# Kernel tuning notes

Hardware: AMD Instinct MI355X
Metric: run time of the kernel (lower is better)

The kernel has to match this reference:

```python
import jax, jax.numpy as jnp
import numpy as np

HID, H, KV, D = 2048, 16, 4, 128
B, L = 8, 1024
T = B * L
EPS = 1e-6
NEG = -1e9


def _rms(x, w):
    # RMSNorm over head_dim in fp32
    var = jnp.mean(x.astype(jnp.float32) ** 2, axis=-1, keepdims=True)
    return (x.astype(jnp.float32) * jax.lax.rsqrt(var + EPS)).astype(x.dtype) * w


def _rot_half(x):
    x1, x2 = jnp.split(x, 2, axis=-1)
    return jnp.concatenate([-x2, x1], axis=-1)


def setup_inputs() -> dict:
    key = jax.random.key(0)
    ks = jax.random.split(key, 24)
    inp = {}
    inp['packed_sequence'] = jax.random.normal(ks[0], (T, HID), jnp.float32) * 0.02
    # RoPE tables: positions restart per sample
    pos = jnp.tile(jnp.arange(L, dtype=jnp.float32), B)  # [T]
    inv_freq = 1.0 / (10000.0 ** (jnp.arange(0, D, 2, dtype=jnp.float32) / D))
    ang = pos[:, None] * inv_freq[None, :]  # [T, D/2]
    inp['cos'] = jnp.concatenate([jnp.cos(ang), jnp.cos(ang)], axis=-1)
    inp['sin'] = jnp.concatenate([jnp.sin(ang), jnp.sin(ang)], axis=-1)
    # per-sample causal additive mask [B, L, L]
    causal = jnp.tril(jnp.ones((L, L), bool))
    inp['attn_bias'] = jnp.broadcast_to(jnp.where(causal, 0.0, NEG).astype(jnp.float32), (B, L, L))
    inp['gen_mask'] = jax.random.randint(ks[1], (T,), 0, 2, jnp.int32)
    s = 0.02
    inp['Wq'] = jax.random.normal(ks[2], (H * D, HID), jnp.float32) * s
    inp['bq'] = jnp.zeros((H * D,), jnp.float32)
    inp['Wqg'] = jax.random.normal(ks[3], (H * D, HID), jnp.float32) * s
    inp['bqg'] = jnp.zeros((H * D,), jnp.float32)
    inp['Wk'] = jax.random.normal(ks[4], (KV * D, HID), jnp.float32) * s
    inp['bk'] = jnp.zeros((KV * D,), jnp.float32)
    inp['Wkg'] = jax.random.normal(ks[5], (KV * D, HID), jnp.float32) * s
    inp['bkg'] = jnp.zeros((KV * D,), jnp.float32)
    inp['Wv'] = jax.random.normal(ks[6], (KV * D, HID), jnp.float32) * s
    inp['bv'] = jnp.zeros((KV * D,), jnp.float32)
    inp['Wvg'] = jax.random.normal(ks[7], (KV * D, HID), jnp.float32) * s
    inp['bvg'] = jnp.zeros((KV * D,), jnp.float32)
    inp['Wo'] = jax.random.normal(ks[8], (HID, H * D), jnp.float32) * s
    inp['Wog'] = jax.random.normal(ks[9], (HID, H * D), jnp.float32) * s
    inp['q_norm_w'] = jnp.ones((D,), jnp.float32)
    inp['q_norm_gen_w'] = jnp.ones((D,), jnp.float32)
    inp['k_norm_w'] = jnp.ones((D,), jnp.float32)
    inp['k_norm_gen_w'] = jnp.ones((D,), jnp.float32)
    return inp


def reference(packed_sequence, cos, sin, attn_bias, gen_mask,
              Wq, bq, Wqg, bqg, Wk, bk, Wkg, bkg, Wv, bv, Wvg, bvg,
              Wo, Wog, q_norm_w, q_norm_gen_w, k_norm_w, k_norm_gen_w):
    route = (gen_mask > 0)[:, None]  # [T,1]; und/gen indexes partition tokens -> select
    # dual-path QKV projections (scatter into zero buffers == per-token select)
    q = jnp.where(route, packed_sequence @ Wqg.T + bqg, packed_sequence @ Wq.T + bq)
    k = jnp.where(route, packed_sequence @ Wkg.T + bkg, packed_sequence @ Wk.T + bk)
    v = jnp.where(route, packed_sequence @ Wvg.T + bvg, packed_sequence @ Wv.T + bv)
    q = q.reshape(T, H, D)
    k = k.reshape(T, KV, D)
    v = v.reshape(T, KV, D)
    rh = route[:, :, None]  # [T,1,1]
    # dual-path per-head-dim RMSNorm
    q = jnp.where(rh, _rms(q, q_norm_gen_w), _rms(q, q_norm_w))
    k = jnp.where(rh, _rms(k, k_norm_gen_w), _rms(k, k_norm_w))
    # RoPE (broadcast over heads, unsqueeze_dim=1)
    c, s = cos[:, None, :], sin[:, None, :]
    q = q * c + _rot_half(q) * s
    k = k * c + _rot_half(k) * s
    # GQA: repeat kv heads to H
    k = jnp.repeat(k, H // KV, axis=1)
    v = jnp.repeat(v, H // KV, axis=1)
    # ragged attention, equal sample lens -> batched SDPA with per-sample masks
    qb = q.reshape(B, L, H, D)
    kb = k.reshape(B, L, H, D)
    vb = v.reshape(B, L, H, D)
    scores = jnp.einsum('blhd,bmhd->bhlm', qb, kb) / np.sqrt(D).astype(np.float32)
    scores = scores + attn_bias[:, None, :, :]
    p = jax.nn.softmax(scores, axis=-1)
    o = jnp.einsum('bhlm,bmhd->blhd', p, vb).reshape(T, H * D)
    # dual-path output projection (no bias)
    return jnp.where(route, o @ Wog.T, o @ Wo.T)
```

## Files before the change

### kernel.cpp

```cpp
#include <hip/hip_runtime.h>

#define T_TOK 8192
#define HID   2048
#define NH    16
#define NKV   4
#define HD    128

typedef __attribute__((ext_vector_type(8))) short short8;
typedef __attribute__((ext_vector_type(4))) float f32x4;
typedef __attribute__((ext_vector_type(4))) unsigned short us4;

__device__ __forceinline__ unsigned short f2b(float f) {
  union { float f; unsigned int u; } x; x.f = f;
  unsigned int u = x.u;
  return (unsigned short)((u + 0x7FFFu + ((u >> 16) & 1u)) >> 16);
}
__device__ __forceinline__ float b2f(unsigned short u) {
  union { float f; unsigned int u; } x; x.u = ((unsigned int)u) << 16; return x.f;
}

__device__ __forceinline__ void ld_lds16(const unsigned short* g, unsigned short* l) {
  __builtin_amdgcn_global_load_lds(
      (const __attribute__((address_space(1))) unsigned int*)g,
      (__attribute__((address_space(3))) unsigned int*)l, 16, 0, 0);
}

__global__ __launch_bounds__(1024) void scan_route(const int* __restrict__ gm,
                                                   int* __restrict__ perm,
                                                   int* __restrict__ n0p) {
  __shared__ int cnt[1024];
  int tid = threadIdx.x;
  int base = tid * 8;
  int r[8]; int c0 = 0;
#pragma unroll
  for (int i = 0; i < 8; i++) { r[i] = gm[base + i] > 0 ? 1 : 0; c0 += 1 - r[i]; }
  cnt[tid] = c0;
  __syncthreads();
  for (int off = 1; off < 1024; off <<= 1) {
    int add = (tid >= off) ? cnt[tid - off] : 0;
    __syncthreads();
    cnt[tid] += add;
    __syncthreads();
  }
  int incl = cnt[tid];
  int total0 = cnt[1023];
  int p0 = incl - c0;
  int p1 = total0 + (base - (incl - c0));
#pragma unroll
  for (int i = 0; i < 8; i++) {
    int t = base + i;
    if (r[i] == 0) perm[p0++] = t;
    else           perm[p1++] = t;
  }
  if (tid == 0) n0p[0] = total0;
}

__global__ __launch_bounds__(256) void convert_bf16(const float* __restrict__ s,
                                                    unsigned short* __restrict__ d,
                                                    int n) {
  int i = (blockIdx.x * 256 + threadIdx.x) * 4;
  if (i >= n) return;
  float4 v = *(const float4*)(s + i);
  us4 o = { f2b(v.x), f2b(v.y), f2b(v.z), f2b(v.w) };
  *(us4*)(d + i) = o;
}

#define BM  128
#define BK  64

__device__ __forceinline__ void gemm_core(
    const unsigned short* __restrict__ Xb,
    const unsigned short* __restrict__ W,
    const float* __restrict__ bias,
    const int* __restrict__ perm,
    int r0, int r1, int col0, int N,
    float* __restrict__ outF, unsigned short* __restrict__ outB,
    unsigned short* As, unsigned short* Bs)
{
  int tid = threadIdx.x;
  int lane = tid & 63, wid = tid >> 6;
  int quad = lane >> 4, l15 = lane & 15;
  int wr = (wid >> 1) * 64, wc = (wid & 1) * 64;
  int lrow = lane >> 3;
  int sc8 = (lane & 7) ^ (lrow & 7);

  const unsigned short* ag[4]; const unsigned short* bg[4];
  unsigned short* al[4]; unsigned short* bl[4];
#pragma unroll
  for (int i = 0; i < 4; i++) {
    int row = wid * 32 + i * 8 + lrow;
    int gr = r0 + row; if (gr > r1 - 1) gr = r1 - 1;
    ag[i] = Xb + (size_t)perm[gr] * HID + sc8 * 8;
    bg[i] = W + (size_t)(col0 + row) * HID + sc8 * 8;
    al[i] = As + (wid * 32 + i * 8) * BK;
    bl[i] = Bs + (wid * 32 + i * 8) * BK;
  }

  f32x4 zero = {0.f, 0.f, 0.f, 0.f};
  f32x4 acc[4][4];
#pragma unroll
  for (int a = 0; a < 4; a++)
#pragma unroll
    for (int b = 0; b < 4; b++) acc[a][b] = zero;

  for (int k0 = 0; k0 < HID; k0 += BK) {
#pragma unroll
    for (int i = 0; i < 4; i++) {
      ld_lds16(ag[i] + k0, al[i]);
      ld_lds16(bg[i] + k0, bl[i]);
    }
    __syncthreads();
#pragma unroll
    for (int kk = 0; kk < 2; kk++) {
      int cswz = ((kk * 4 + quad) ^ (l15 & 7)) * 8;
      short8 af[4], bf[4];
#pragma unroll
      for (int mt = 0; mt < 4; mt++)
        af[mt] = *(const short8*)&As[(wr + mt * 16 + l15) * BK + cswz];
#pragma unroll
      for (int nt = 0; nt < 4; nt++)
        bf[nt] = *(const short8*)&Bs[(wc + nt * 16 + l15) * BK + cswz];
#pragma unroll
      for (int mt = 0; mt < 4; mt++)
#pragma unroll
        for (int nt = 0; nt < 4; nt++)
          acc[mt][nt] = __builtin_amdgcn_mfma_f32_16x16x32_bf16(af[mt], bf[nt], acc[mt][nt], 0, 0, 0);
    }
    __syncthreads();
  }

#pragma unroll
  for (int mt = 0; mt < 4; mt++) {
#pragma unroll
    for (int r = 0; r < 4; r++) {
      int lr = wr + mt * 16 + quad * 4 + r;
      int gr = r0 + lr;
      if (gr >= r1) continue;
      int tok = perm[gr];
#pragma unroll
      for (int nt = 0; nt < 4; nt++) {
        int col = col0 + wc + nt * 16 + l15;
        float v = acc[mt][nt][r];
        if (bias) v += bias[col];
        if (outF) outF[(size_t)tok * N + col] = v;
        else      outB[(size_t)tok * N + col] = f2b(v);
      }
    }
  }
}

__global__ __launch_bounds__(256, 3) void gemm_qkv(
    const unsigned short* __restrict__ xb,
    const unsigned short* wq0, const unsigned short* wq1,
    const float* bq0, const float* bq1,
    const unsigned short* wk0, const unsigned short* wk1,
    const float* bk0, const float* bk1,
    const unsigned short* wv0, const unsigned short* wv1,
    const float* bv0, const float* bv1,
    unsigned short* qraw, unsigned short* kraw, unsigned short* vb,
    const int* __restrict__ perm, const int* __restrict__ n0p)
{
  __shared__ unsigned short As[BM * BK];
  __shared__ unsigned short Bs[BM * BK];
  int set = blockIdx.z;
  int n0 = n0p[0];
  int r0, r1;
  if (set == 0) { r0 = blockIdx.x * BM; if (r0 >= n0) return; r1 = (r0 + BM < n0) ? r0 + BM : n0; }
  else          { r0 = n0 + blockIdx.x * BM; if (r0 >= T_TOK) return; r1 = (r0 + BM < T_TOK) ? r0 + BM : T_TOK; }
  int y = blockIdx.y;
  const unsigned short* w; const float* bias;
  unsigned short* ob; int col0, N;
  if (y < 16)      { w = set ? wq1 : wq0; bias = set ? bq1 : bq0; col0 = y * 128;        N = HID; ob = qraw; }
  else if (y < 20) { w = set ? wk1 : wk0; bias = set ? bk1 : bk0; col0 = (y - 16) * 128; N = 512; ob = kraw; }
  else             { w = set ? wv1 : wv0; bias = set ? bv1 : bv0; col0 = (y - 20) * 128; N = 512; ob = vb; }
  gemm_core(xb, w, bias, perm, r0, r1, col0, N, nullptr, ob, As, Bs);
}

__global__ __launch_bounds__(256, 3) void gemm_out(
    const unsigned short* __restrict__ obuf,
    const unsigned short* wo0, const unsigned short* wo1,
    float* __restrict__ out,
    const int* __restrict__ perm, const int* __restrict__ n0p)
{
  __shared__ unsigned short As[BM * BK];
  __shared__ unsigned short Bs[BM * BK];
  int set = blockIdx.z;
  int n0 = n0p[0];
  int r0, r1;
  if (set == 0) { r0 = blockIdx.x * BM; if (r0 >= n0) return; r1 = (r0 + BM < n0) ? r0 + BM : n0; }
  else          { r0 = n0 + blockIdx.x * BM; if (r0 >= T_TOK) return; r1 = (r0 + BM < T_TOK) ? r0 + BM : T_TOK; }
  gemm_core(obuf, set ? wo1 : wo0, nullptr, perm, r0, r1, blockIdx.y * 128, HID, out, nullptr, As, Bs);
}

__global__ __launch_bounds__(256) void rms_rope(
    const unsigned short* __restrict__ in, unsigned short* __restrict__ outp,
    const float* __restrict__ cosb, const float* __restrict__ sinb,
    const int* __restrict__ gm,
    const float* __restrict__ wn, const float* __restrict__ wg, int nh)
{
  int wvid = blockIdx.x * 4 + (threadIdx.x >> 6);
  int lane = threadIdx.x & 63;
  int t = wvid / nh, h = wvid - t * nh;
  size_t off = ((size_t)t * nh + h) * HD;
  float x1 = b2f(in[off + lane]), x2 = b2f(in[off + 64 + lane]);
  float ss = x1 * x1 + x2 * x2;
#pragma unroll
  for (int o = 32; o > 0; o >>= 1) ss += __shfl_xor(ss, o, 64);
  float inv = rsqrtf(ss * (1.0f / 128.0f) + 1e-6f);
  const float* w = (gm[t] > 0) ? wg : wn;
  float n1 = x1 * inv * w[lane];
  float n2 = x2 * inv * w[lane + 64];
  float c1 = cosb[t * HD + lane],      s1 = sinb[t * HD + lane];
  float c2 = cosb[t * HD + 64 + lane], s2 = sinb[t * HD + 64 + lane];
  outp[off + lane]      = f2b(n1 * c1 - n2 * s1);
  outp[off + 64 + lane] = f2b(n2 * c2 + n1 * s2);
}

__global__ __launch_bounds__(256, 2) void attn_kernel(
    const unsigned short* __restrict__ qb,
    const unsigned short* __restrict__ kb,
    const unsigned short* __restrict__ vb,
    unsigned short* __restrict__ ob)
{
  __shared__ unsigned short Ks[64 * 136];
  __shared__ unsigned short Vt[128 * 72];
  __shared__ unsigned short Ps[4 * 16 * 72];
  int pslot = blockIdx.x, kvh = blockIdx.y, b = blockIdx.z;
  int tid = threadIdx.x, lane = tid & 63, wid = tid >> 6, quad = lane >> 4, l15 = lane & 15;
  int h = kvh * 4 + wid;
  const float sc = 0.088388347648318447f;
  f32x4 zero = {0.f, 0.f, 0.f, 0.f};

  for (int half = 0; half < 2; half++) {
    int a = half ? (31 - pslot) : pslot;
    int q0 = a * 32;
    short8 qfr[2][4];
#pragma unroll
    for (int g = 0; g < 2; g++) {
      size_t qoff = ((size_t)(b * 1024 + q0 + g * 16 + l15) * NH + h) * HD;
#pragma unroll
      for (int kk = 0; kk < 4; kk++)
        qfr[g][kk] = *(const short8*)(qb + qoff + kk * 32 + quad * 8);
    }
    f32x4 oacc[2][8];
#pragma unroll
    for (int g = 0; g < 2; g++)
#pragma unroll
      for (int i = 0; i < 8; i++) oacc[g][i] = zero;
    float lpart[2][4] = {{0.f,0.f,0.f,0.f},{0.f,0.f,0.f,0.f}};

    int ktiles = a / 2 + 1;
    for (int kt = 0; kt < ktiles; kt++) {
      int kv0 = kt * 64;
      __syncthreads();
#pragma unroll
      for (int i = 0; i < 4; i++) {
        int idx = tid + i * 256;
        int key = idx >> 4, cc = idx & 15;
        *(short8*)&Ks[key * 136 + cc * 8] =
            *(const short8*)(kb + ((size_t)(b * 1024 + kv0 + key) * NKV + kvh) * HD + cc * 8);
      }
      {
        int key = tid & 63;
#pragma unroll
        for (int i = 0; i < 4; i++) {
          int cc = (tid >> 6) + i * 4;
          short8 v = *(const short8*)(vb + ((size_t)(b * 1024 + kv0 + key) * NKV + kvh) * HD + cc * 8);
#pragma unroll
          for (int j = 0; j < 8; j++) Vt[(cc * 8 + j) * 72 + key] = (unsigned short)v[j];
        }
      }
      __syncthreads();
      bool lastt = (kt == ktiles - 1);
#pragma unroll
      for (int g = 0; g < 2; g++) {
        f32x4 s[4];
#pragma unroll
        for (int g4 = 0; g4 < 4; g4++) {
          f32x4 acc = zero;
#pragma unroll
          for (int kk = 0; kk < 4; kk++) {
            short8 bfr = *(const short8*)&Ks[(g4 * 16 + l15) * 136 + kk * 32 + quad * 8];
            acc = __builtin_amdgcn_mfma_f32_16x16x32_bf16(qfr[g][kk], bfr, acc, 0, 0, 0);
          }
          s[g4] = acc;
        }
        int rowb = q0 + g * 16 + quad * 4;
#pragma unroll
        for (int g4 = 0; g4 < 4; g4++) {
          int col = kv0 + g4 * 16 + l15;
#pragma unroll
          for (int r = 0; r < 4; r++) {
            float p = __expf(s[g4][r] * sc);
            if (lastt && col > rowb + r) p = 0.f;
            lpart[g][r] += p;
            Ps[wid * 1152 + (quad * 4 + r) * 72 + g4 * 16 + l15] = f2b(p);
          }
        }
#pragma unroll
        for (int kk = 0; kk < 2; kk++) {
          short8 pa = *(const short8*)&Ps[wid * 1152 + l15 * 72 + kk * 32 + quad * 8];
#pragma unroll
          for (int dg = 0; dg < 8; dg++) {
            short8 vf = *(const short8*)&Vt[(dg * 16 + l15) * 72 + kk * 32 + quad * 8];
            oacc[g][dg] = __builtin_amdgcn_mfma_f32_16x16x32_bf16(pa, vf, oacc[g][dg], 0, 0, 0);
          }
        }
      }
    }
#pragma unroll
    for (int g = 0; g < 2; g++) {
#pragma unroll
      for (int r = 0; r < 4; r++) {
        float v = lpart[g][r];
#pragma unroll
        for (int o = 8; o > 0; o >>= 1) v += __shfl_xor(v, o, 64);
        lpart[g][r] = 1.0f / v;
      }
#pragma unroll
      for (int dg = 0; dg < 8; dg++)
#pragma unroll
        for (int r = 0; r < 4; r++) {
          int row = q0 + g * 16 + quad * 4 + r;
          ob[((size_t)(b * 1024 + row) * NH + h) * HD + dg * 16 + l15] =
              f2b(oacc[g][dg][r] * lpart[g][r]);
        }
    }
  }
}

extern "C" void kernel_launch(void* const* d_in, const int* in_sizes, int n_in,
                              void* d_out, int out_size, void* d_ws, size_t ws_size,
                              hipStream_t stream) {
  const float* x    = (const float*)d_in[0];
  const float* cosb = (const float*)d_in[1];
  const float* sinb = (const float*)d_in[2];
  const int*   gm   = (const int*)d_in[4];
  const float* Wq   = (const float*)d_in[5];
  const float* bq   = (const float*)d_in[6];
  const float* Wqg  = (const float*)d_in[7];
  const float* bqg  = (const float*)d_in[8];
  const float* Wk   = (const float*)d_in[9];
  const float* bk   = (const float*)d_in[10];
  const float* Wkg  = (const float*)d_in[11];
  const float* bkg  = (const float*)d_in[12];
  const float* Wv   = (const float*)d_in[13];
  const float* bv   = (const float*)d_in[14];
  const float* Wvg  = (const float*)d_in[15];
  const float* bvg  = (const float*)d_in[16];
  const float* Wo   = (const float*)d_in[17];
  const float* Wog  = (const float*)d_in[18];
  const float* qnw  = (const float*)d_in[19];
  const float* qngw = (const float*)d_in[20];
  const float* knw  = (const float*)d_in[21];
  const float* kngw = (const float*)d_in[22];
  float* out = (float*)d_out;

  char* wsb = (char*)d_ws;
  size_t off = 0;
  auto alloc = [&](size_t bytes) -> char* {
    char* p = wsb + off;
    off += (bytes + 255) & ~(size_t)255;
    return p;
  };
  int* perm = (int*)alloc((size_t)T_TOK * 4);
  int* n0p  = (int*)alloc(4);
  unsigned short* xb  = (unsigned short*)alloc((size_t)T_TOK * HID * 2);
  unsigned short* wq0 = (unsigned short*)alloc((size_t)HID * HID * 2);
  unsigned short* wq1 = (unsigned short*)alloc((size_t)HID * HID * 2);
  unsigned short* wk0 = (unsigned short*)alloc((size_t)512 * HID * 2);
  unsigned short* wk1 = (unsigned short*)alloc((size_t)512 * HID * 2);
  unsigned short* wv0 = (unsigned short*)alloc((size_t)512 * HID * 2);
  unsigned short* wv1 = (unsigned short*)alloc((size_t)512 * HID * 2);
  unsigned short* wo0 = (unsigned short*)alloc((size_t)HID * HID * 2);
  unsigned short* wo1 = (unsigned short*)alloc((size_t)HID * HID * 2);
  unsigned short* qraw = (unsigned short*)alloc((size_t)T_TOK * HID * 2);
  unsigned short* kraw = (unsigned short*)alloc((size_t)T_TOK * 512 * 2);
  unsigned short* vbuf = (unsigned short*)alloc((size_t)T_TOK * 512 * 2);
  unsigned short* qbuf = (unsigned short*)alloc((size_t)T_TOK * HID * 2);
  unsigned short* kbuf = (unsigned short*)alloc((size_t)T_TOK * 512 * 2);
  unsigned short* obuf = qraw;

  scan_route<<<dim3(1), dim3(1024), 0, stream>>>(gm, perm, n0p);

  auto conv = [&](const float* s, unsigned short* d, int n) {
    convert_bf16<<<dim3(n / 1024), dim3(256), 0, stream>>>(s, d, n);
  };
  conv(x,   xb,  T_TOK * HID);
  conv(Wq,  wq0, HID * HID);  conv(Wqg, wq1, HID * HID);
  conv(Wk,  wk0, 512 * HID);  conv(Wkg, wk1, 512 * HID);
  conv(Wv,  wv0, 512 * HID);  conv(Wvg, wv1, 512 * HID);
  conv(Wo,  wo0, HID * HID);  conv(Wog, wo1, HID * HID);

  gemm_qkv<<<dim3(64, 24, 2), dim3(256), 0, stream>>>(
      xb, wq0, wq1, bq, bqg, wk0, wk1, bk, bkg, wv0, wv1, bv, bvg,
      qraw, kraw, vbuf, perm, n0p);

  rms_rope<<<dim3(T_TOK * NH / 4), dim3(256), 0, stream>>>(
      qraw, qbuf, cosb, sinb, gm, qnw, qngw, NH);
  rms_rope<<<dim3(T_TOK * NKV / 4), dim3(256), 0, stream>>>(
      kraw, kbuf, cosb, sinb, gm, knw, kngw, NKV);

  attn_kernel<<<dim3(16, 4, 8), dim3(256), 0, stream>>>(qbuf, kbuf, vbuf, obuf);

  gemm_out<<<dim3(64, 16, 2), dim3(256), 0, stream>>>(obuf, wo0, wo1, out, perm, n0p);
}
```

Before: 629.1 us.

## Merge bf16 conversions, pre-transpose V, and restructure attention with swizzled async LDS

The nine fp32-to-bf16 conversion launches become one kernel that finds its source and destination from a block-offset table, removing launch overhead. A new kernel writes V transposed to global memory, so the attention kernel loads K and V tiles straight into LDS with global_load_lds instead of doing a scalar transpose in LDS. The attention block grows to 512 threads, with each wave handling one 16-row query group. K, V and P in LDS use XOR swizzling in place of padding to avoid bank conflicts. In exchange there is an extra kernel and an extra global buffer for V, and a larger block that may hurt occupancy.

```diff
diff --git a/kernel.cpp b/kernel.cpp
--- a/kernel.cpp
+++ b/kernel.cpp
@@ -55,14 +55,21 @@
   if (tid == 0) n0p[0] = total0;
 }
 
-__global__ __launch_bounds__(256) void convert_bf16(const float* __restrict__ s,
-                                                    unsigned short* __restrict__ d,
-                                                    int n) {
-  int i = (blockIdx.x * 256 + threadIdx.x) * 4;
-  if (i >= n) return;
-  float4 v = *(const float4*)(s + i);
+struct ConvArgs {
+  const float* src[9];
+  unsigned short* dst[9];
+  int blk_end[9];
+};
+
+__global__ __launch_bounds__(256) void convert_all(ConvArgs a) {
+  int blk = blockIdx.x;
+  int s = 0;
+  while (blk >= a.blk_end[s]) s++;
+  int local = blk - (s ? a.blk_end[s - 1] : 0);
+  int i = local * 1024 + threadIdx.x * 4;
+  float4 v = *(const float4*)(a.src[s] + i);
   us4 o = { f2b(v.x), f2b(v.y), f2b(v.z), f2b(v.w) };
-  *(us4*)(d + i) = o;
+  *(us4*)(a.dst[s] + i) = o;
 }
 
 #define BM  128
@@ -216,116 +223,137 @@
   outp[off + 64 + lane] = f2b(n2 * c2 + n1 * s2);
 }
 
-__global__ __launch_bounds__(256, 2) void attn_kernel(
+__global__ __launch_bounds__(256) void vtrans(const unsigned short* __restrict__ vb,
+                                              unsigned short* __restrict__ vt) {
+  __shared__ unsigned short Vs[64][136];
+  int kt = blockIdx.x, kvh = blockIdx.y, b = blockIdx.z;
+  int t = threadIdx.x;
+  int kv0 = kt * 64;
+  int key = t >> 2, c0 = t & 3;
+#pragma unroll
+  for (int i = 0; i < 4; i++) {
+    int cc = c0 * 4 + i;
+    *(short8*)&Vs[key][cc * 8] =
+        *(const short8*)(vb + ((size_t)(b * 1024 + kv0 + key) * NKV + kvh) * HD + cc * 8);
+  }
+  __syncthreads();
+  int d = t >> 1, hh = t & 1;
+  unsigned short tmp[32];
+#pragma unroll
+  for (int k = 0; k < 32; k++) tmp[k] = Vs[hh * 32 + k][d];
+  size_t base = ((size_t)(b * NKV + kvh) * HD + d) * 1024 + kv0 + hh * 32;
+  *(short8*)(vt + base)      = *(short8*)&tmp[0];
+  *(short8*)(vt + base + 8)  = *(short8*)&tmp[8];
+  *(short8*)(vt + base + 16) = *(short8*)&tmp[16];
+  *(short8*)(vt + base + 24) = *(short8*)&tmp[24];
+}
+
+__global__ __launch_bounds__(512, 2) void attn_kernel(
     const unsigned short* __restrict__ qb,
     const unsigned short* __restrict__ kb,
-    const unsigned short* __restrict__ vb,
+    const unsigned short* __restrict__ vt,
     unsigned short* __restrict__ ob)
 {
-  __shared__ unsigned short Ks[64 * 136];
-  __shared__ unsigned short Vt[128 * 72];
-  __shared__ unsigned short Ps[4 * 16 * 72];
+  __shared__ unsigned short Ks[64 * 128];
+  __shared__ unsigned short Vt[128 * 64];
+  __shared__ unsigned short Ps[8 * 16 * 64];
   int pslot = blockIdx.x, kvh = blockIdx.y, b = blockIdx.z;
-  int tid = threadIdx.x, lane = tid & 63, wid = tid >> 6, quad = lane >> 4, l15 = lane & 15;
-  int h = kvh * 4 + wid;
+  int tid = threadIdx.x, lane = tid & 63, wid = tid >> 6;
+  int quad = lane >> 4, l15 = lane & 15;
+  int h = kvh * 4 + (wid >> 1);
+  int g = wid & 1;
   const float sc = 0.088388347648318447f;
   f32x4 zero = {0.f, 0.f, 0.f, 0.f};
+
+  int skey = (wid << 2) + (lane >> 4);
+  int kswz = ((lane & 15) ^ (skey & 7)) * 8;
+  int sd   = (wid << 3) + (lane >> 3);
+  int vswz = ((lane & 7) ^ (sd & 7)) * 8;
 
   for (int half = 0; half < 2; half++) {
     int a = half ? (31 - pslot) : pslot;
     int q0 = a * 32;
-    short8 qfr[2][4];
-#pragma unroll
-    for (int g = 0; g < 2; g++) {
-      size_t qoff = ((size_t)(b * 1024 + q0 + g * 16 + l15) * NH + h) * HD;
-#pragma unroll
-      for (int kk = 0; kk < 4; kk++)
-        qfr[g][kk] = *(const short8*)(qb + qoff + kk * 32 + quad * 8);
-    }
-    f32x4 oacc[2][8];
-#pragma unroll
-    for (int g = 0; g < 2; g++)
-#pragma unroll
-      for (int i = 0; i < 8; i++) oacc[g][i] = zero;
-    float lpart[2][4] = {{0.f,0.f,0.f,0.f},{0.f,0.f,0.f,0.f}};
+    int qrow = q0 + g * 16 + l15;
+    size_t qoff = ((size_t)(b * 1024 + qrow) * NH + h) * HD;
+    short8 qfr[4];
+#pragma unroll
+    for (int kk = 0; kk < 4; kk++)
+      qfr[kk] = *(const short8*)(qb + qoff + kk * 32 + quad * 8);
+
+    f32x4 oacc[8];
+#pragma unroll
+    for (int i = 0; i < 8; i++) oacc[i] = zero;
+    float lpart[4] = {0.f, 0.f, 0.f, 0.f};
 
     int ktiles = a / 2 + 1;
     for (int kt = 0; kt < ktiles; kt++) {
       int kv0 = kt * 64;
       __syncthreads();
 #pragma unroll
-      for (int i = 0; i < 4; i++) {
-        int idx = tid + i * 256;
-        int key = idx >> 4, cc = idx & 15;
-        *(short8*)&Ks[key * 136 + cc * 8] =
-            *(const short8*)(kb + ((size_t)(b * 1024 + kv0 + key) * NKV + kvh) * HD + cc * 8);
-      }
-      {
-        int key = tid & 63;
-#pragma unroll
-        for (int i = 0; i < 4; i++) {
-          int cc = (tid >> 6) + i * 4;
-          short8 v = *(const short8*)(vb + ((size_t)(b * 1024 + kv0 + key) * NKV + kvh) * HD + cc * 8);
-#pragma unroll
-          for (int j = 0; j < 8; j++) Vt[(cc * 8 + j) * 72 + key] = (unsigned short)v[j];
-        }
+      for (int i = 0; i < 2; i++) {
+        int key = i * 32 + skey;
+        ld_lds16(kb + ((size_t)(b * 1024 + kv0 + key) * NKV + kvh) * HD + kswz,
+                 Ks + (size_t)(i * 32 + (wid << 2)) * 128);
+      }
+#pragma unroll
+      for (int i = 0; i < 2; i++) {
+        int d = i * 64 + sd;
+        ld_lds16(vt + ((size_t)(b * NKV + kvh) * HD + d) * 1024 + kv0 + vswz,
+                 Vt + (size_t)(i * 64 + (wid << 3)) * 64);
       }
       __syncthreads();
       bool lastt = (kt == ktiles - 1);
-#pragma unroll
-      for (int g = 0; g < 2; g++) {
-        f32x4 s[4];
-#pragma unroll
-        for (int g4 = 0; g4 < 4; g4++) {
-          f32x4 acc = zero;
-#pragma unroll
-          for (int kk = 0; kk < 4; kk++) {
-            short8 bfr = *(const short8*)&Ks[(g4 * 16 + l15) * 136 + kk * 32 + quad * 8];
-            acc = __builtin_amdgcn_mfma_f32_16x16x32_bf16(qfr[g][kk], bfr, acc, 0, 0, 0);
-          }
-          s[g4] = acc;
+
+      f32x4 s[4];
+#pragma unroll
+      for (int g4 = 0; g4 < 4; g4++) {
+        f32x4 acc = zero;
+#pragma unroll
+        for (int kk = 0; kk < 4; kk++) {
+          short8 bfr = *(const short8*)&Ks[(g4 * 16 + l15) * 128 + ((kk * 4 + quad) ^ (l15 & 7)) * 8];
+          acc = __builtin_amdgcn_mfma_f32_16x16x32_bf16(qfr[kk], bfr, acc, 0, 0, 0);
         }
-        int rowb = q0 + g * 16 + quad * 4;
-#pragma unroll
-        for (int g4 = 0; g4 < 4; g4++) {
-          int col = kv0 + g4 * 16 + l15;
-#pragma unroll
-          for (int r = 0; r < 4; r++) {
-            float p = __expf(s[g4][r] * sc);
-            if (lastt && col > rowb + r) p = 0.f;
-            lpart[g][r] += p;
-            Ps[wid * 1152 + (quad * 4 + r) * 72 + g4 * 16 + l15] = f2b(p);
-          }
+        s[g4] = acc;
+      }
+      int rowb = q0 + g * 16 + quad * 4;
+#pragma unroll
+      for (int g4 = 0; g4 < 4; g4++) {
+        int col = kv0 + g4 * 16 + l15;
+        int k8 = g4 * 2 + (l15 >> 3);
+#pragma unroll
+        for (int r = 0; r < 4; r++) {
+          float p = __expf(s[g4][r] * sc);
+          if (lastt && col > rowb + r) p = 0.f;
+          lpart[r] += p;
+          int row = quad * 4 + r;
+          Ps[wid * 1024 + row * 64 + ((k8 ^ (row & 7)) * 8 + (l15 & 7))] = f2b(p);
         }
-#pragma unroll
-        for (int kk = 0; kk < 2; kk++) {
-          short8 pa = *(const short8*)&Ps[wid * 1152 + l15 * 72 + kk * 32 + quad * 8];
-#pragma unroll
-          for (int dg = 0; dg < 8; dg++) {
-            short8 vf = *(const short8*)&Vt[(dg * 16 + l15) * 72 + kk * 32 + quad * 8];
-            oacc[g][dg] = __builtin_amdgcn_mfma_f32_16x16x32_bf16(pa, vf, oacc[g][dg], 0, 0, 0);
-          }
+      }
+#pragma unroll
+      for (int kk = 0; kk < 2; kk++) {
+        short8 pa = *(const short8*)&Ps[wid * 1024 + l15 * 64 + ((kk * 4 + quad) ^ (l15 & 7)) * 8];
+#pragma unroll
+        for (int dg = 0; dg < 8; dg++) {
+          short8 vf = *(const short8*)&Vt[(dg * 16 + l15) * 64 + ((kk * 4 + quad) ^ (l15 & 7)) * 8];
+          oacc[dg] = __builtin_amdgcn_mfma_f32_16x16x32_bf16(pa, vf, oacc[dg], 0, 0, 0);
         }
       }
     }
 #pragma unroll
-    for (int g = 0; g < 2; g++) {
+    for (int r = 0; r < 4; r++) {
+      float v = lpart[r];
+#pragma unroll
+      for (int o = 8; o > 0; o >>= 1) v += __shfl_xor(v, o, 64);
+      lpart[r] = 1.0f / v;
+    }
+#pragma unroll
+    for (int dg = 0; dg < 8; dg++)
 #pragma unroll
       for (int r = 0; r < 4; r++) {
-        float v = lpart[g][r];
-#pragma unroll
-        for (int o = 8; o > 0; o >>= 1) v += __shfl_xor(v, o, 64);
-        lpart[g][r] = 1.0f / v;
-      }
-#pragma unroll
-      for (int dg = 0; dg < 8; dg++)
-#pragma unroll
-        for (int r = 0; r < 4; r++) {
-          int row = q0 + g * 16 + quad * 4 + r;
-          ob[((size_t)(b * 1024 + row) * NH + h) * HD + dg * 16 + l15] =
-              f2b(oacc[g][dg][r] * lpart[g][r]);
-        }
-    }
+        int row = q0 + g * 16 + quad * 4 + r;
+        ob[((size_t)(b * 1024 + row) * NH + h) * HD + dg * 16 + l15] =
+            f2b(oacc[dg][r] * lpart[r]);
+      }
   }
 }
 
@@ -377,20 +405,24 @@
   unsigned short* qraw = (unsigned short*)alloc((size_t)T_TOK * HID * 2);
   unsigned short* kraw = (unsigned short*)alloc((size_t)T_TOK * 512 * 2);
   unsigned short* vbuf = (unsigned short*)alloc((size_t)T_TOK * 512 * 2);
+  unsigned short* vtb  = (unsigned short*)alloc((size_t)T_TOK * 512 * 2);
   unsigned short* qbuf = (unsigned short*)alloc((size_t)T_TOK * HID * 2);
   unsigned short* kbuf = (unsigned short*)alloc((size_t)T_TOK * 512 * 2);
   unsigned short* obuf = qraw;
 
   scan_route<<<dim3(1), dim3(1024), 0, stream>>>(gm, perm, n0p);
 
-  auto conv = [&](const float* s, unsigned short* d, int n) {
-    convert_bf16<<<dim3(n / 1024), dim3(256), 0, stream>>>(s, d, n);
-  };
-  conv(x,   xb,  T_TOK * HID);
-  conv(Wq,  wq0, HID * HID);  conv(Wqg, wq1, HID * HID);
-  conv(Wk,  wk0, 512 * HID);  conv(Wkg, wk1, 512 * HID);
-  conv(Wv,  wv0, 512 * HID);  conv(Wvg, wv1, 512 * HID);
-  conv(Wo,  wo0, HID * HID);  conv(Wog, wo1, HID * HID);
+  ConvArgs ca;
+  const float* srcs[9] = {x, Wq, Wqg, Wk, Wkg, Wv, Wvg, Wo, Wog};
+  unsigned short* dsts[9] = {xb, wq0, wq1, wk0, wk1, wv0, wv1, wo0, wo1};
+  int ns[9] = {T_TOK * HID, HID * HID, HID * HID, 512 * HID, 512 * HID,
+               512 * HID, 512 * HID, HID * HID, HID * HID};
+  int cum = 0;
+  for (int i = 0; i < 9; i++) {
+    ca.src[i] = srcs[i]; ca.dst[i] = dsts[i];
+    cum += ns[i] / 1024; ca.blk_end[i] = cum;
+  }
+  convert_all<<<dim3(cum), dim3(256), 0, stream>>>(ca);
 
   gemm_qkv<<<dim3(64, 24, 2), dim3(256), 0, stream>>>(
       xb, wq0, wq1, bq, bqg, wk0, wk1, bk, bkg, wv0, wv1, bv, bvg,
@@ -400,8 +432,9 @@
       qraw, qbuf, cosb, sinb, gm, qnw, qngw, NH);
   rms_rope<<<dim3(T_TOK * NKV / 4), dim3(256), 0, stream>>>(
       kraw, kbuf, cosb, sinb, gm, knw, kngw, NKV);
-
-  attn_kernel<<<dim3(16, 4, 8), dim3(256), 0, stream>>>(qbuf, kbuf, vbuf, obuf);
+  vtrans<<<dim3(16, 4, 8), dim3(256), 0, stream>>>(vbuf, vtb);
+
+  attn_kernel<<<dim3(16, 4, 8), dim3(512), 0, stream>>>(qbuf, kbuf, vtb, obuf);
 
   gemm_out<<<dim3(64, 16, 2), dim3(256), 0, stream>>>(obuf, wo0, wo1, out, perm, n0p);
 }
```

Measured after the change: 591.7 us. -5.9%, faster.
